# Kernel optimization log

Measured on AMD Instinct MI355X. Metric: run time of the kernel, lower is better.

## Reference

```python
import jax, jax.numpy as jnp
import numpy as np
from jax import lax

B, T, D, H = 256, 1024, 128, 256

def setup_inputs() -> dict:
    key = jax.random.key(0)
    ks = jax.random.split(key, 12)
    s_gate = 1.0 / np.sqrt(D + H)
    s_head = 1.0 / np.sqrt(2 * H)
    return {
        "x": jax.random.normal(ks[0], (B, T, D), jnp.float32),
        "Wi": jax.random.uniform(ks[1], (H, D + H), jnp.float32, -s_gate, s_gate),
        "bi": jax.random.uniform(ks[2], (H,), jnp.float32, -s_gate, s_gate),
        "Wf": jax.random.uniform(ks[3], (H, D + H), jnp.float32, -s_gate, s_gate),
        "bf": jax.random.uniform(ks[4], (H,), jnp.float32, -s_gate, s_gate),
        "Wo": jax.random.uniform(ks[5], (H, D + H), jnp.float32, -s_gate, s_gate),
        "bo": jax.random.uniform(ks[6], (H,), jnp.float32, -s_gate, s_gate),
        "Wc": jax.random.uniform(ks[7], (H, D + H), jnp.float32, -s_gate, s_gate),
        "bc": jax.random.uniform(ks[8], (H,), jnp.float32, -s_gate, s_gate),
        "W2": jax.random.uniform(ks[9], (1, 2 * H), jnp.float32, -s_head, s_head),
        "b2": jax.random.uniform(ks[10], (1,), jnp.float32, -s_head, s_head),
    }

def reference(x, Wi, bi, Wf, bf, Wo, bo, Wc, bc, W2, b2):
    # x: [B, T, D] -> scan over time dim
    xs = jnp.transpose(x, (1, 0, 2))  # [T, B, D]
    b, h = xs.shape[1], Wi.shape[0]
    h0 = jnp.zeros((b, h), x.dtype)
    c0 = jnp.zeros((b, h), x.dtype)

    def step(carry, xt):
        hid, cov = carry
        comb = jnp.concatenate([xt, hid], axis=1)  # [B, D+H]
        i = jax.nn.sigmoid(comb @ Wi.T + bi)
        f = jax.nn.sigmoid(comb @ Wf.T + bf)
        o = jax.nn.sigmoid(comb @ Wo.T + bo)
        c_tilde = jnp.tanh(comb @ Wc.T + bc)
        cov = f * cov + i * c_tilde
        hid = o * jnp.tanh(cov)
        return (hid, cov), None

    (hid, cov), _ = lax.scan(step, (h0, c0), xs)
    out = jax.nn.sigmoid(jnp.concatenate([hid, cov], axis=1) @ W2.T + b2)  # [B, 1]
    return out, hid
```

## Files before the change

kernel.cpp:

```cpp
#include <hip/hip_runtime.h>
#include <hip/hip_fp16.h>


typedef _Float16 half8 __attribute__((ext_vector_type(8)));
typedef float f32x4 __attribute__((ext_vector_type(4)));

#define MFMA16(a, b, c) __builtin_amdgcn_mfma_f32_16x16x32_f16((a), (b), (c), 0, 0, 0)

__device__ __forceinline__ float2 h2f2(unsigned int u) {
  __half2 h;
  __builtin_memcpy(&h, &u, 4);
  return __half22float2(h);
}

__device__ __forceinline__ float lstm_elem(float a_i, float a_f, float a_o, float a_c,
                                           float& c) {
  float eA = __expf(-fminf(fmaxf(a_i, -40.f), 40.f));
  float eC = __expf(2.f * fminf(fmaxf(a_c, -15.f), 15.f));
  float ict = (eC - 1.f) * __builtin_amdgcn_rcpf((1.f + eA) * (eC + 1.f));
  float eF = __expf(-fminf(fmaxf(a_f, -40.f), 40.f));
  float fg = __builtin_amdgcn_rcpf(1.f + eF);
  float cv = fg * c + ict;
  c = cv;
  float eO = __expf(-fminf(fmaxf(a_o, -40.f), 40.f));
  float eV = __expf(2.f * fminf(fmaxf(cv, -15.f), 15.f));
  return (eV - 1.f) * __builtin_amdgcn_rcpf((1.f + eO) * (eV + 1.f));
}

__global__ void w16_kernel(const float* __restrict__ Wi, const float* __restrict__ Wf,
                           const float* __restrict__ Wo, const float* __restrict__ Wc,
                           __half* __restrict__ w16x)
{
  int g = blockIdx.x, c = threadIdx.x;
  int q = g >> 8;
  const float* Wq = (q == 0) ? Wi : (q == 1) ? Wf : (q == 2) ? Wo : Wc;
  w16x[g * 128 + c] = __float2half_rn(Wq[(size_t)(g & 255) * 384 + c]);
}

__global__ __launch_bounds__(256) void gx_kernel(
    const __half* __restrict__ w16x,
    const float* __restrict__ bi, const float* __restrict__ bf,
    const float* __restrict__ bo, const float* __restrict__ bc,
    const float* __restrict__ x, unsigned* __restrict__ gx, int t0)
{
  const int tid = threadIdx.x;
  const int l = tid & 63, wv = tid >> 6;
  const int kq = l >> 4, col = l & 15;
  const int tch = blockIdx.x, bg = blockIdx.y, gh = blockIdx.z;
  const size_t brow = (size_t)(bg * 16 + col);
  const int bg8 = bg * 2 + (kq >> 1);
  const int lclo = (kq & 1) * 16 + col;

#pragma unroll
  for (int mh = 0; mh < 2; ++mh) {
    half8 afr[4][4];
#pragma unroll
    for (int mm = 0; mm < 4; ++mm) {
      int tt = t0 + tch * 8 + mh * 4 + mm;
      const float* xp = x + (brow * 1024 + tt) * 128 + kq * 8;
#pragma unroll
      for (int k = 0; k < 4; ++k) {
        float4 a = *(const float4*)(xp + k * 32);
        float4 b = *(const float4*)(xp + k * 32 + 4);
        afr[mm][k] = {(_Float16)a.x, (_Float16)a.y, (_Float16)a.z, (_Float16)a.w,
                      (_Float16)b.x, (_Float16)b.y, (_Float16)b.z, (_Float16)b.w};
      }
    }
#pragma unroll
    for (int n = 0; n < 8; ++n) {
      int gbase = gh * 512 + wv * 128 + n * 16;
      int gcol = gbase + col;
      int q = gcol >> 8;
      const float* Bq = (q == 0) ? bi : (q == 1) ? bf : (q == 2) ? bo : bc;
      float bv = Bq[gcol & 255];
      half8 wf[4];
#pragma unroll
      for (int k = 0; k < 4; ++k)
        wf[k] = *(const half8*)(w16x + (size_t)(gbase + col) * 128 + k * 32 + kq * 8);
      int qg = gbase >> 8;
      int t16 = (gbase >> 4) & 15;
#pragma unroll
      for (int mm = 0; mm < 4; ++mm) {
        f32x4 acc = {bv, bv, bv, bv};
#pragma unroll
        for (int k = 0; k < 4; ++k) acc = MFMA16(afr[mm][k], wf[k], acc);
        int tl = tch * 8 + mh * 4 + mm;
        unsigned lo = (unsigned)__half_as_ushort(__float2half_rn(acc[0])) |
                      ((unsigned)__half_as_ushort(__float2half_rn(acc[1])) << 16);
        unsigned hi = (unsigned)__half_as_ushort(__float2half_rn(acc[2])) |
                      ((unsigned)__half_as_ushort(__float2half_rn(acc[3])) << 16);
        unsigned* gp = gx + ((((size_t)tl * 32 + bg8) * 16 + t16) * 4 + qg) * 64;
        gp[lclo] = lo;
        gp[32 + lclo] = hi;
      }
    }
  }
}

#define NFV 46

#define WFRAG(ctl, q, k)                                                      \
  ((((ctl) * 4 + (q)) * 8 + (k)) < NFV                                        \
       ? wfr[(((ctl) * 4 + (q)) * 8 + (k))]                                   \
       : *(const half8*)(WL + ((((ctl) * 4 + (q)) * 8 + (k)) - NFV) * 1024 + lofs))

__global__ __launch_bounds__(512) __attribute__((amdgpu_waves_per_eu(2, 2)))
void rec_kernel(
    const float* __restrict__ Wi, const float* __restrict__ Wf,
    const float* __restrict__ Wo, const float* __restrict__ Wc,
    const unsigned* __restrict__ gx, float* __restrict__ dout,
    float* __restrict__ c_plain, float* __restrict__ c_state,
    __half* __restrict__ h_state, int t0, int tc)
{
  __shared__ char lds[163840];
  const int tid = threadIdx.x;
  const int l = tid & 63, w = tid >> 6;
  const int kq = l >> 4, col = l & 15;
  const int lofs = l * 16;
  const int bg8 = blockIdx.x;
  char* WL = lds + w * 18432;
  char* HF = lds + 147456;

  half8 wfr[NFV];
#pragma unroll
  for (int ctl = 0; ctl < 2; ++ctl) {
#pragma unroll
    for (int q = 0; q < 4; ++q) {
      const float* Wq = (q == 0) ? Wi : (q == 1) ? Wf : (q == 2) ? Wo : Wc;
      int j = (w * 2 + ctl) * 16 + col;
      const float* src = Wq + (size_t)j * 384 + 128 + kq * 8;
#pragma unroll
      for (int k = 0; k < 8; ++k) {
        float4 a = *(const float4*)(src + k * 32);
        float4 b = *(const float4*)(src + k * 32 + 4);
        half8 h = {(_Float16)a.x, (_Float16)a.y, (_Float16)a.z, (_Float16)a.w,
                   (_Float16)b.x, (_Float16)b.y, (_Float16)b.z, (_Float16)b.w};
        int i = (ctl * 4 + q) * 8 + k;
        if (i < NFV)
          wfr[i] = h;
        else
          *(half8*)(WL + (i - NFV) * 1024 + lofs) = h;
      }
    }
  }

  {
    uint4 z = {0, 0, 0, 0};
    *(uint4*)(HF + (tid >> 8) * 8192 + 4096 + (tid & 255) * 16) = z;
  }
  float cst[4];
  if (t0 == 0) {
#pragma unroll
    for (int i = 0; i < 4; ++i) cst[i] = 0.f;
    uint2 z2 = {0, 0};
    *(uint2*)(HF + tid * 8) = z2;
  } else {
#pragma unroll
    for (int i = 0; i < 4; ++i) cst[i] = c_state[(size_t)bg8 * 2048 + tid * 4 + i];
    int r8 = tid >> 6, c4 = tid & 63;
    uint2 v = *(const uint2*)(h_state + (size_t)bg8 * 2048 + r8 * 256 + c4 * 4);
    *(uint2*)(HF + ((t0 & 1) << 13) + r8 * 512 + ((c4 * 8) ^ ((r8 & 7) << 4))) = v;
  }

  const char* gxw = (const char*)gx + ((size_t)bg8 * 16 + w * 2) * 1024 + l * 4;
  unsigned gxv[8];
#pragma unroll
  for (int c = 0; c < 8; ++c)
    gxv[c] = *(const unsigned*)(gxw + (c >> 2) * 1024 + (c & 3) * 256);

  const int rswz = (l & 7) << 4;
  const int rbase = (l & 15) * 512;
  const int hi5 = (l >> 5);
  const int baddr = (l & 31) * 4;

  for (int tt = 0; tt < tc; ++tt) {
    const int s = t0 + tt;
    const char* rb = HF + ((s & 1) << 13);
    char* wb = HF + (((s & 1) ^ 1) << 13);
    __syncthreads();
    const bool lastT = (s == 1023);
    const bool endC = (tt + 1 == tc);
    const char* gxn = gxw + (size_t)((tt + 1 < tc) ? tt + 1 : tt) * 524288;

#pragma unroll
    for (int ctl = 0; ctl < 2; ++ctl) {
      f32x4 acc[4] = {{0.f, 0.f, 0.f, 0.f}, {0.f, 0.f, 0.f, 0.f},
                      {0.f, 0.f, 0.f, 0.f}, {0.f, 0.f, 0.f, 0.f}};
#pragma unroll
      for (int kh = 0; kh < 2; ++kh) {
        half8 afr[4];
#pragma unroll
        for (int k2 = 0; k2 < 4; ++k2)
          afr[k2] = *(const half8*)(rb + rbase + (((kh * 4 + k2) * 64 + kq * 16) ^ rswz));
#pragma unroll
        for (int k2 = 0; k2 < 4; ++k2) {
          acc[0] = MFMA16(afr[k2], WFRAG(ctl, 0, kh * 4 + k2), acc[0]);
          acc[1] = MFMA16(afr[k2], WFRAG(ctl, 1, kh * 4 + k2), acc[1]);
          acc[2] = MFMA16(afr[k2], WFRAG(ctl, 2, kh * 4 + k2), acc[2]);
          acc[3] = MFMA16(afr[k2], WFRAG(ctl, 3, kh * 4 + k2), acc[3]);
        }
      }
      float P0[4], P1[4];
#pragma unroll
      for (int q = 0; q < 4; ++q) {
        int r0 = __builtin_amdgcn_ds_bpermute(baddr, __float_as_int(acc[q][0]));
        int r1 = __builtin_amdgcn_ds_bpermute(baddr, __float_as_int(acc[q][1]));
        int r2 = __builtin_amdgcn_ds_bpermute(baddr, __float_as_int(acc[q][2]));
        int r3 = __builtin_amdgcn_ds_bpermute(baddr, __float_as_int(acc[q][3]));
        P0[q] = __int_as_float(hi5 ? r2 : r0);
        P1[q] = __int_as_float(hi5 ? r3 : r1);
      }
#pragma unroll
      for (int q = 0; q < 4; ++q) {
        float2 g = h2f2(gxv[ctl * 4 + q]);
        P0[q] += g.x;
        P1[q] += g.y;
      }
      const int j2 = (w * 2 + ctl) * 16 + col;
      const int rowb = (kq & 1) * 4 + hi5 * 2;
      {
        float hv = lstm_elem(P0[0], P0[1], P0[2], P0[3], cst[ctl * 2 + 0]);
        int row = rowb;
        *(_Float16*)(wb + row * 512 + ((j2 * 2) ^ ((row & 7) << 4))) = (_Float16)hv;
        if (lastT) {
          int rrow = bg8 * 8 + row;
          dout[256 + (size_t)rrow * 256 + j2] = hv;
          c_plain[(size_t)rrow * 256 + j2] = cst[ctl * 2 + 0];
        } else if (endC) {
          h_state[(size_t)bg8 * 2048 + row * 256 + j2] = __float2half_rn(hv);
        }
      }
      {
        float hv = lstm_elem(P1[0], P1[1], P1[2], P1[3], cst[ctl * 2 + 1]);
        int row = rowb + 1;
        *(_Float16*)(wb + row * 512 + ((j2 * 2) ^ ((row & 7) << 4))) = (_Float16)hv;
        if (lastT) {
          int rrow = bg8 * 8 + row;
          dout[256 + (size_t)rrow * 256 + j2] = hv;
          c_plain[(size_t)rrow * 256 + j2] = cst[ctl * 2 + 1];
        } else if (endC) {
          h_state[(size_t)bg8 * 2048 + row * 256 + j2] = __float2half_rn(hv);
        }
      }
#pragma unroll
      for (int q = 0; q < 4; ++q)
        gxv[ctl * 4 + q] = *(const unsigned*)(gxn + ctl * 1024 + q * 256);
    }
  }

#pragma unroll
  for (int i = 0; i < 4; ++i) c_state[(size_t)bg8 * 2048 + tid * 4 + i] = cst[i];
}

__global__ void head_kernel(const float* __restrict__ hid, const float* __restrict__ cpl,
                            const float* __restrict__ W2, const float* __restrict__ b2,
                            float* __restrict__ out)
{
  int b = blockIdx.x, l = threadIdx.x;
  float4 hv = ((const float4*)(hid + (size_t)b * 256))[l];
  float4 wv = ((const float4*)W2)[l];
  float s = hv.x * wv.x + hv.y * wv.y + hv.z * wv.z + hv.w * wv.w;
  float4 cv = ((const float4*)(cpl + (size_t)b * 256))[l];
  float4 wc = ((const float4*)(W2 + 256))[l];
  s += cv.x * wc.x + cv.y * wc.y + cv.z * wc.z + cv.w * wc.w;
#pragma unroll
  for (int off = 32; off > 0; off >>= 1) s += __shfl_down(s, off, 64);
  if (l == 0) out[b] = 1.f / (1.f + __expf(-(s + b2[0])));
}

extern "C" void kernel_launch(void* const* d_in, const int* in_sizes, int n_in,
                              void* d_out, int out_size, void* d_ws, size_t ws_size,
                              hipStream_t stream)
{
  const float* x  = (const float*)d_in[0];
  const float* Wi = (const float*)d_in[1];
  const float* bi = (const float*)d_in[2];
  const float* Wf = (const float*)d_in[3];
  const float* bf = (const float*)d_in[4];
  const float* Wo = (const float*)d_in[5];
  const float* bo = (const float*)d_in[6];
  const float* Wc = (const float*)d_in[7];
  const float* bc = (const float*)d_in[8];
  const float* W2 = (const float*)d_in[9];
  const float* b2 = (const float*)d_in[10];
  float* out = (float*)d_out;

  char* ws = (char*)d_ws;
  const size_t state_bytes = (size_t)896 * 1024;
  size_t avail = ws_size > state_bytes ? ws_size - state_bytes : 0;
  size_t tcap = avail / 524288;
  int TC = (int)(tcap > 1024 ? 1024 : (tcap & ~(size_t)7));
  if (TC < 8) TC = 8;
  unsigned* gxb = (unsigned*)ws;
  float* c_plain = (float*)(ws + (size_t)TC * 524288);
  float* c_state = c_plain + 65536;
  __half* h_state = (__half*)(c_state + 65536);
  __half* w16x = (__half*)(h_state + 65536);

  w16_kernel<<<1024, 128, 0, stream>>>(Wi, Wf, Wo, Wc, w16x);
  for (int t0 = 0; t0 < 1024; t0 += TC) {
    int tcn = (1024 - t0 < TC) ? (1024 - t0) : TC;
    gx_kernel<<<dim3(tcn / 8, 16, 2), 256, 0, stream>>>(w16x, bi, bf, bo, bc, x, gxb, t0);
    rec_kernel<<<32, 512, 0, stream>>>(Wi, Wf, Wo, Wc, gxb, out, c_plain, c_state,
                                       h_state, t0, tcn);
  }
  head_kernel<<<256, 64, 0, stream>>>(out + 256, c_plain, W2, b2, out);
}
```

Measured before the change: 3.485 ms.

## Drop bpermute transposes by relaying out gx and computing gates in MFMA layout

Changes the gx precompute layout so each lane of the recurrent kernel loads its four gate pre-activations with vectorized uint4 loads matching the MFMA accumulator layout. The ds_bpermute shuffles are removed, and only lanes 0-31 (which hold valid rows) write h and c. The two ctl halves are merged into one k-loop that shares each A-fragment load across 8 MFMAs. The gx prefetch for the next step is gone and gx is loaded at the start of each step instead, which may expose global latency. Half the lanes now compute throwaway LSTM math, and the cell state grows from 4 to 8 floats per thread.

```diff
diff --git a/kernel.cpp b/kernel.cpp
--- a/kernel.cpp
+++ b/kernel.cpp
@@ -49,7 +49,7 @@
   const int tch = blockIdx.x, bg = blockIdx.y, gh = blockIdx.z;
   const size_t brow = (size_t)(bg * 16 + col);
   const int bg8 = bg * 2 + (kq >> 1);
-  const int lclo = (kq & 1) * 16 + col;
+  const int kqc = kq & 1;
 
 #pragma unroll
   for (int mh = 0; mh < 2; ++mh) {
@@ -77,8 +77,9 @@
 #pragma unroll
       for (int k = 0; k < 4; ++k)
         wf[k] = *(const half8*)(w16x + (size_t)(gbase + col) * 128 + k * 32 + kq * 8);
-      int qg = gbase >> 8;
-      int t16 = (gbase >> 4) & 15;
+      int gt = gbase >> 4;
+      int qg = gt >> 4;
+      int wc = (gt & 15) >> 1, ctlc = gt & 1;
 #pragma unroll
       for (int mm = 0; mm < 4; ++mm) {
         f32x4 acc = {bv, bv, bv, bv};
@@ -89,9 +90,10 @@
                       ((unsigned)__half_as_ushort(__float2half_rn(acc[1])) << 16);
         unsigned hi = (unsigned)__half_as_ushort(__float2half_rn(acc[2])) |
                       ((unsigned)__half_as_ushort(__float2half_rn(acc[3])) << 16);
-        unsigned* gp = gx + ((((size_t)tl * 32 + bg8) * 16 + t16) * 4 + qg) * 64;
-        gp[lclo] = lo;
-        gp[32 + lclo] = hi;
+        unsigned* gp = gx + (((((size_t)tl * 32 + bg8) * 8 + wc) * 4 + qg) * 16 + col) * 8 +
+                       kqc * 4 + ctlc * 2;
+        uint2 v = {lo, hi};
+        *(uint2*)gp = v;
       }
     }
   }
@@ -99,10 +101,10 @@
 
 #define NFV 46
 
-#define WFRAG(ctl, q, k)                                                      \
-  ((((ctl) * 4 + (q)) * 8 + (k)) < NFV                                        \
-       ? wfr[(((ctl) * 4 + (q)) * 8 + (k))]                                   \
-       : *(const half8*)(WL + ((((ctl) * 4 + (q)) * 8 + (k)) - NFV) * 1024 + lofs))
+#define WFRAG(ctl, q, kk)                                                     \
+  ((((ctl) * 4 + (q)) * 8 + (kk)) < NFV                                       \
+       ? wfr[(((ctl) * 4 + (q)) * 8 + (kk))]                                  \
+       : *(const half8*)(WL + ((((ctl) * 4 + (q)) * 8 + (kk)) - NFV) * 1024 + lofs))
 
 __global__ __launch_bounds__(512) __attribute__((amdgpu_waves_per_eu(2, 2)))
 void rec_kernel(
@@ -116,6 +118,7 @@
   const int tid = threadIdx.x;
   const int l = tid & 63, w = tid >> 6;
   const int kq = l >> 4, col = l & 15;
+  const int ll = l & 31;
   const int lofs = l * 16;
   const int bg8 = blockIdx.x;
   char* WL = lds + w * 18432;
@@ -130,12 +133,12 @@
       int j = (w * 2 + ctl) * 16 + col;
       const float* src = Wq + (size_t)j * 384 + 128 + kq * 8;
 #pragma unroll
-      for (int k = 0; k < 8; ++k) {
-        float4 a = *(const float4*)(src + k * 32);
-        float4 b = *(const float4*)(src + k * 32 + 4);
+      for (int kk = 0; kk < 8; ++kk) {
+        float4 a = *(const float4*)(src + kk * 32);
+        float4 b = *(const float4*)(src + kk * 32 + 4);
         half8 h = {(_Float16)a.x, (_Float16)a.y, (_Float16)a.z, (_Float16)a.w,
                    (_Float16)b.x, (_Float16)b.y, (_Float16)b.z, (_Float16)b.w};
-        int i = (ctl * 4 + q) * 8 + k;
+        int i = (ctl * 4 + q) * 8 + kk;
         if (i < NFV)
           wfr[i] = h;
         else
@@ -148,108 +151,120 @@
     uint4 z = {0, 0, 0, 0};
     *(uint4*)(HF + (tid >> 8) * 8192 + 4096 + (tid & 255) * 16) = z;
   }
-  float cst[4];
+  float cst[8];
+  const bool act = (l < 32);
   if (t0 == 0) {
 #pragma unroll
-    for (int i = 0; i < 4; ++i) cst[i] = 0.f;
+    for (int i = 0; i < 8; ++i) cst[i] = 0.f;
     uint2 z2 = {0, 0};
     *(uint2*)(HF + tid * 8) = z2;
   } else {
-#pragma unroll
-    for (int i = 0; i < 4; ++i) cst[i] = c_state[(size_t)bg8 * 2048 + tid * 4 + i];
+    if (act) {
+#pragma unroll
+      for (int ctl = 0; ctl < 2; ++ctl)
+#pragma unroll
+        for (int rg = 0; rg < 4; ++rg) {
+          int row = (ll >> 4) * 4 + rg;
+          int j2 = (w * 2 + ctl) * 16 + (ll & 15);
+          cst[ctl * 4 + rg] = c_state[(size_t)bg8 * 2048 + row * 256 + j2];
+        }
+    } else {
+#pragma unroll
+      for (int i = 0; i < 8; ++i) cst[i] = 0.f;
+    }
     int r8 = tid >> 6, c4 = tid & 63;
     uint2 v = *(const uint2*)(h_state + (size_t)bg8 * 2048 + r8 * 256 + c4 * 4);
     *(uint2*)(HF + ((t0 & 1) << 13) + r8 * 512 + ((c4 * 8) ^ ((r8 & 7) << 4))) = v;
   }
-
-  const char* gxw = (const char*)gx + ((size_t)bg8 * 16 + w * 2) * 1024 + l * 4;
-  unsigned gxv[8];
-#pragma unroll
-  for (int c = 0; c < 8; ++c)
-    gxv[c] = *(const unsigned*)(gxw + (c >> 2) * 1024 + (c & 3) * 256);
+  __syncthreads();
+
+  const char* gxb = (const char*)gx + ((size_t)bg8 * 8 + w) * 2048 +
+                    (ll & 15) * 32 + (ll >> 4) * 16;
 
   const int rswz = (l & 7) << 4;
   const int rbase = (l & 15) * 512;
-  const int hi5 = (l >> 5);
-  const int baddr = (l & 31) * 4;
 
   for (int tt = 0; tt < tc; ++tt) {
     const int s = t0 + tt;
     const char* rb = HF + ((s & 1) << 13);
     char* wb = HF + (((s & 1) ^ 1) << 13);
     __syncthreads();
+
+    const char* gxs = gxb + (size_t)tt * 524288;
+    uint4 gxq[4];
+#pragma unroll
+    for (int q = 0; q < 4; ++q) gxq[q] = *(const uint4*)(gxs + q * 512);
+
+    f32x4 acc[2][4] = {{{0.f, 0.f, 0.f, 0.f}, {0.f, 0.f, 0.f, 0.f},
+                        {0.f, 0.f, 0.f, 0.f}, {0.f, 0.f, 0.f, 0.f}},
+                       {{0.f, 0.f, 0.f, 0.f}, {0.f, 0.f, 0.f, 0.f},
+                        {0.f, 0.f, 0.f, 0.f}, {0.f, 0.f, 0.f, 0.f}}};
+#pragma unroll
+    for (int kk = 0; kk < 8; ++kk) {
+      half8 afr = *(const half8*)(rb + rbase + ((kk * 64 + kq * 16) ^ rswz));
+      acc[0][0] = MFMA16(afr, WFRAG(0, 0, kk), acc[0][0]);
+      acc[0][1] = MFMA16(afr, WFRAG(0, 1, kk), acc[0][1]);
+      acc[0][2] = MFMA16(afr, WFRAG(0, 2, kk), acc[0][2]);
+      acc[0][3] = MFMA16(afr, WFRAG(0, 3, kk), acc[0][3]);
+      acc[1][0] = MFMA16(afr, WFRAG(1, 0, kk), acc[1][0]);
+      acc[1][1] = MFMA16(afr, WFRAG(1, 1, kk), acc[1][1]);
+      acc[1][2] = MFMA16(afr, WFRAG(1, 2, kk), acc[1][2]);
+      acc[1][3] = MFMA16(afr, WFRAG(1, 3, kk), acc[1][3]);
+    }
+
     const bool lastT = (s == 1023);
     const bool endC = (tt + 1 == tc);
-    const char* gxn = gxw + (size_t)((tt + 1 < tc) ? tt + 1 : tt) * 524288;
 
 #pragma unroll
     for (int ctl = 0; ctl < 2; ++ctl) {
-      f32x4 acc[4] = {{0.f, 0.f, 0.f, 0.f}, {0.f, 0.f, 0.f, 0.f},
-                      {0.f, 0.f, 0.f, 0.f}, {0.f, 0.f, 0.f, 0.f}};
-#pragma unroll
-      for (int kh = 0; kh < 2; ++kh) {
-        half8 afr[4];
-#pragma unroll
-        for (int k2 = 0; k2 < 4; ++k2)
-          afr[k2] = *(const half8*)(rb + rbase + (((kh * 4 + k2) * 64 + kq * 16) ^ rswz));
-#pragma unroll
-        for (int k2 = 0; k2 < 4; ++k2) {
-          acc[0] = MFMA16(afr[k2], WFRAG(ctl, 0, kh * 4 + k2), acc[0]);
-          acc[1] = MFMA16(afr[k2], WFRAG(ctl, 1, kh * 4 + k2), acc[1]);
-          acc[2] = MFMA16(afr[k2], WFRAG(ctl, 2, kh * 4 + k2), acc[2]);
-          acc[3] = MFMA16(afr[k2], WFRAG(ctl, 3, kh * 4 + k2), acc[3]);
+      float gI[4], gF[4], gO[4], gC[4];
+      {
+        float2 a = h2f2(gxq[0][ctl * 2]), b = h2f2(gxq[0][ctl * 2 + 1]);
+        gI[0] = a.x; gI[1] = a.y; gI[2] = b.x; gI[3] = b.y;
+      }
+      {
+        float2 a = h2f2(gxq[1][ctl * 2]), b = h2f2(gxq[1][ctl * 2 + 1]);
+        gF[0] = a.x; gF[1] = a.y; gF[2] = b.x; gF[3] = b.y;
+      }
+      {
+        float2 a = h2f2(gxq[2][ctl * 2]), b = h2f2(gxq[2][ctl * 2 + 1]);
+        gO[0] = a.x; gO[1] = a.y; gO[2] = b.x; gO[3] = b.y;
+      }
+      {
+        float2 a = h2f2(gxq[3][ctl * 2]), b = h2f2(gxq[3][ctl * 2 + 1]);
+        gC[0] = a.x; gC[1] = a.y; gC[2] = b.x; gC[3] = b.y;
+      }
+      const int j2 = (w * 2 + ctl) * 16 + (ll & 15);
+#pragma unroll
+      for (int rg = 0; rg < 4; ++rg) {
+        float hv = lstm_elem(acc[ctl][0][rg] + gI[rg], acc[ctl][1][rg] + gF[rg],
+                             acc[ctl][2][rg] + gO[rg], acc[ctl][3][rg] + gC[rg],
+                             cst[ctl * 4 + rg]);
+        if (act) {
+          int row = (ll >> 4) * 4 + rg;
+          *(_Float16*)(wb + row * 512 + ((j2 * 2) ^ ((row & 7) << 4))) = (_Float16)hv;
+          if (lastT) {
+            int rrow = bg8 * 8 + row;
+            dout[256 + (size_t)rrow * 256 + j2] = hv;
+            c_plain[(size_t)rrow * 256 + j2] = cst[ctl * 4 + rg];
+          } else if (endC) {
+            h_state[(size_t)bg8 * 2048 + row * 256 + j2] = __float2half_rn(hv);
+          }
         }
       }
-      float P0[4], P1[4];
-#pragma unroll
-      for (int q = 0; q < 4; ++q) {
-        int r0 = __builtin_amdgcn_ds_bpermute(baddr, __float_as_int(acc[q][0]));
-        int r1 = __builtin_amdgcn_ds_bpermute(baddr, __float_as_int(acc[q][1]));
-        int r2 = __builtin_amdgcn_ds_bpermute(baddr, __float_as_int(acc[q][2]));
-        int r3 = __builtin_amdgcn_ds_bpermute(baddr, __float_as_int(acc[q][3]));
-        P0[q] = __int_as_float(hi5 ? r2 : r0);
-        P1[q] = __int_as_float(hi5 ? r3 : r1);
-      }
-#pragma unroll
-      for (int q = 0; q < 4; ++q) {
-        float2 g = h2f2(gxv[ctl * 4 + q]);
-        P0[q] += g.x;
-        P1[q] += g.y;
-      }
-      const int j2 = (w * 2 + ctl) * 16 + col;
-      const int rowb = (kq & 1) * 4 + hi5 * 2;
-      {
-        float hv = lstm_elem(P0[0], P0[1], P0[2], P0[3], cst[ctl * 2 + 0]);
-        int row = rowb;
-        *(_Float16*)(wb + row * 512 + ((j2 * 2) ^ ((row & 7) << 4))) = (_Float16)hv;
-        if (lastT) {
-          int rrow = bg8 * 8 + row;
-          dout[256 + (size_t)rrow * 256 + j2] = hv;
-          c_plain[(size_t)rrow * 256 + j2] = cst[ctl * 2 + 0];
-        } else if (endC) {
-          h_state[(size_t)bg8 * 2048 + row * 256 + j2] = __float2half_rn(hv);
-        }
-      }
-      {
-        float hv = lstm_elem(P1[0], P1[1], P1[2], P1[3], cst[ctl * 2 + 1]);
-        int row = rowb + 1;
-        *(_Float16*)(wb + row * 512 + ((j2 * 2) ^ ((row & 7) << 4))) = (_Float16)hv;
-        if (lastT) {
-          int rrow = bg8 * 8 + row;
-          dout[256 + (size_t)rrow * 256 + j2] = hv;
-          c_plain[(size_t)rrow * 256 + j2] = cst[ctl * 2 + 1];
-        } else if (endC) {
-          h_state[(size_t)bg8 * 2048 + row * 256 + j2] = __float2half_rn(hv);
-        }
-      }
-#pragma unroll
-      for (int q = 0; q < 4; ++q)
-        gxv[ctl * 4 + q] = *(const unsigned*)(gxn + ctl * 1024 + q * 256);
-    }
-  }
-
-#pragma unroll
-  for (int i = 0; i < 4; ++i) c_state[(size_t)bg8 * 2048 + tid * 4 + i] = cst[i];
+    }
+  }
+
+  if (act) {
+#pragma unroll
+    for (int ctl = 0; ctl < 2; ++ctl)
+#pragma unroll
+      for (int rg = 0; rg < 4; ++rg) {
+        int row = (ll >> 4) * 4 + rg;
+        int j2 = (w * 2 + ctl) * 16 + (ll & 15);
+        c_state[(size_t)bg8 * 2048 + row * 256 + j2] = cst[ctl * 4 + rg];
+      }
+  }
 }
 
 __global__ void head_kernel(const float* __restrict__ hid, const float* __restrict__ cpl,
```

Measured after the change: 4.567 ms. 31.1% more time.
